# Performance work log

Hardware: AMD Instinct MI355X
Metric: run time of the kernel (lower is better)

The kernel has to match this reference:

```python
import jax, jax.numpy as jnp
import numpy as np

ALPHA = 1.702
LIMIT = 7.0


def setup_inputs() -> dict:
    key = jax.random.key(0)
    ks = jax.random.split(key, 6)
    T, H, D, E = 8192, 1024, 1024, 8
    hidden_states = jax.random.normal(ks[0], (T, H), dtype=jnp.float32)
    routing_weights = jax.random.uniform(ks[1], (T, E), dtype=jnp.float32)
    # 0.02 scale keeps activations in a sane range (original uses raw randn params)
    gate_up_proj = jax.random.normal(ks[2], (E, H, 2 * D), dtype=jnp.float32) * 0.02
    gate_up_proj_bias = jax.random.normal(ks[3], (E, 2 * D), dtype=jnp.float32) * 0.02
    down_proj = jax.random.normal(ks[4], (E, D, H), dtype=jnp.float32) * 0.02
    down_proj_bias = jax.random.normal(ks[5], (E, H), dtype=jnp.float32) * 0.02
    return {
        "hidden_states": hidden_states,
        "routing_weights": routing_weights,
        "gate_up_proj": gate_up_proj,
        "gate_up_proj_bias": gate_up_proj_bias,
        "down_proj": down_proj,
        "down_proj_bias": down_proj_bias,
    }


def reference(hidden_states, routing_weights, gate_up_proj, gate_up_proj_bias,
              down_proj, down_proj_bias):
    # hidden_states: [T, H]; routing_weights: [T, E] (batch_size == T in the torch code)
    B, H = hidden_states.shape[0], hidden_states.shape[-1]
    hs = hidden_states.reshape(-1, H)  # [T, H]
    # all-experts batched GEMM: [E, T, 2D]
    gate_up = jnp.einsum('th,ehd->etd', hs, gate_up_proj) + gate_up_proj_bias[:, None, :]
    gate = jnp.minimum(gate_up[..., ::2], LIMIT)          # [E, T, D]
    up = jnp.clip(gate_up[..., 1::2], -LIMIT, LIMIT)      # [E, T, D]
    glu = gate * jax.nn.sigmoid(gate * ALPHA)
    # down projection: [E, T, H]
    next_states = jnp.einsum('etd,edh->eth', (up + 1.0) * glu, down_proj) \
        + down_proj_bias[:, None, :]
    # routing-weighted combine over experts: [T, H]
    out = jnp.einsum('eth,te->th', next_states, routing_weights)
    return out.reshape(B, -1, H)  # [T, 1, H], matching final .view(batch_size, -1, hidden)
```

## Files before the change

kernel.cpp:

```cpp
#include <hip/hip_runtime.h>
#include <hip/hip_bf16.h>

#define T_DIM 8192
#define H_DIM 1024
#define D_DIM 1024
#define E_DIM 8
#define TWO_D 2048
#define K2 8192

#define ALPHA_C 1.702f
#define LIMIT_C 7.0f

typedef __attribute__((ext_vector_type(8))) short s8v;
typedef __attribute__((ext_vector_type(4))) float f4v;

__device__ __forceinline__ void g2l16(const void* g, void* l) {
    __builtin_amdgcn_global_load_lds((const __attribute__((address_space(1))) void*)g,
                                     (__attribute__((address_space(3))) void*)l, 16, 0, 0);
}

__device__ __forceinline__ unsigned short f2bf(float f) {
    __hip_bfloat16 h = __float2bfloat16(f);
    return __builtin_bit_cast(unsigned short, h);
}


__global__ void f32_to_bf16_kernel(const float* __restrict__ in,
                                   unsigned short* __restrict__ out, size_t n) {
    size_t i = ((size_t)blockIdx.x * blockDim.x + threadIdx.x) * 4;
    if (i + 3 < n) {
        float4 v = *(const float4*)(in + i);
        ushort4 o;
        o.x = f2bf(v.x); o.y = f2bf(v.y); o.z = f2bf(v.z); o.w = f2bf(v.w);
        *(ushort4*)(out + i) = o;
    }
}

__global__ void transpose_conv_kernel(const float* __restrict__ in,
                                      unsigned short* __restrict__ out,
                                      int cols, size_t ibs, size_t obs, size_t ors,
                                      int remap) {
    __shared__ float t[32][33];
    const int b = blockIdx.z;
    const int c0 = blockIdx.x * 32, r0 = blockIdx.y * 32;
    const int tx = threadIdx.x & 31, ty = threadIdx.x >> 5;
    const float* ip = in + (size_t)b * ibs;
    #pragma unroll
    for (int i = 0; i < 4; ++i)
        t[ty + i * 8][tx] = ip[(size_t)(r0 + ty + i * 8) * cols + c0 + tx];
    __syncthreads();
    unsigned short* op = out + (size_t)b * obs;
    #pragma unroll
    for (int i = 0; i < 4; ++i) {
        int c = c0 + ty + i * 8;
        int nc = remap ? ((c & ~31) + ((c & 1) << 4) + ((c >> 1) & 15)) : c;
        op[(size_t)nc * ors + r0 + tx] = f2bf(t[tx][ty + i * 8]);
    }
}


__global__ __launch_bounds__(256, 2) void gemm1_kernel(
    const short* __restrict__ Ag0,
    const short* __restrict__ Bg0,
    const float* __restrict__ b1,
    const float* __restrict__ rw,
    __hip_bfloat16* __restrict__ act2)
{
    const int e = blockIdx.z;
    const int mBase = blockIdx.x * 128;
    const int nBase = blockIdx.y * 128;
    const int tid = threadIdx.x;
    const int lane = tid & 63;
    const int wave = tid >> 6;
    const int wm = wave >> 1, wn = wave & 1;
    const int cq = lane & 15, quad = lane >> 4;

    __shared__ __align__(16) short As[128 * 64];
    __shared__ __align__(16) short Bs[128 * 64];

    const short* Ag = Ag0 + (size_t)mBase * H_DIM;
    const short* Bg = Bg0 + ((size_t)e * TWO_D + nBase) * H_DIM;

    f4v acc[4][4];
    #pragma unroll
    for (int mt = 0; mt < 4; ++mt)
        #pragma unroll
        for (int nt = 0; nt < 4; ++nt)
            acc[mt][nt] = (f4v){0.f, 0.f, 0.f, 0.f};

    const int srow8 = lane >> 3;
    const int gco = ((lane & 7) ^ srow8) * 8;
    const int cq7 = cq & 7;

    for (int k0 = 0; k0 < H_DIM; k0 += 64) {
        #pragma unroll
        for (int i = 0; i < 4; ++i) {
            const int r = wave * 32 + i * 8 + srow8;
            g2l16(Ag + (size_t)r * H_DIM + k0 + gco, As + (wave * 32 + i * 8) * 64);
            g2l16(Bg + (size_t)r * H_DIM + k0 + gco, Bs + (wave * 32 + i * 8) * 64);
        }
        __syncthreads();
        #pragma unroll
        for (int h = 0; h < 2; ++h) {
            s8v af[4], bf[4];
            const int pc = (((h << 2) + quad) ^ cq7) * 8;
            #pragma unroll
            for (int i = 0; i < 4; ++i) {
                af[i] = *(const s8v*)(As + (wm * 64 + i * 16 + cq) * 64 + pc);
                bf[i] = *(const s8v*)(Bs + (wn * 64 + i * 16 + cq) * 64 + pc);
            }
            #pragma unroll
            for (int mt = 0; mt < 4; ++mt)
                #pragma unroll
                for (int nt = 0; nt < 4; ++nt)
                    acc[mt][nt] = __builtin_amdgcn_mfma_f32_16x16x32_bf16(
                        af[mt], bf[nt], acc[mt][nt], 0, 0, 0);
        }
        __syncthreads();
    }

    float rwv[4][4];
    #pragma unroll
    for (int mt = 0; mt < 4; ++mt)
        #pragma unroll
        for (int r = 0; r < 4; ++r)
            rwv[mt][r] = rw[(size_t)(mBase + wm * 64 + mt * 16 + quad * 4 + r) * E_DIM + e];

    #pragma unroll
    for (int p = 0; p < 2; ++p) {
        const int j = (((nBase + wn * 64 + p * 32) >> 5) << 4) + cq;
        const float gb = b1[(size_t)e * TWO_D + 2 * j];
        const float ub = b1[(size_t)e * TWO_D + 2 * j + 1];
        #pragma unroll
        for (int mt = 0; mt < 4; ++mt) {
            #pragma unroll
            for (int r = 0; r < 4; ++r) {
                float gate = acc[mt][2 * p][r] + gb;
                float up   = acc[mt][2 * p + 1][r] + ub;
                gate = fminf(gate, LIMIT_C);
                up = fminf(fmaxf(up, -LIMIT_C), LIMIT_C);
                float glu = gate / (1.f + __expf(-ALPHA_C * gate));
                float a = (up + 1.f) * glu * rwv[mt][r];
                const int row = mBase + wm * 64 + mt * 16 + quad * 4 + r;
                act2[(size_t)row * K2 + (size_t)e * D_DIM + j] = __float2bfloat16(a);
            }
        }
    }
}


#define FEN asm volatile("" ::: "memory")
#define BARR { FEN; __builtin_amdgcn_s_barrier(); FEN; }
#define VMW0 asm volatile("s_waitcnt vmcnt(0)" ::: "memory")

__global__ __launch_bounds__(256, 2) void gemm2_kernel(
    const short* __restrict__ Ag0,
    const short* __restrict__ Bg0,
    const float* __restrict__ rw,
    const float* __restrict__ b3,
    float* __restrict__ out)
{
    const int id = blockIdx.x;
    const int mBase = (id & 63) * 128;
    const int nBase = (id >> 6) * 128;
    const int tid = threadIdx.x;
    const int lane = tid & 63;
    const int wave = tid >> 6;
    const int wm = wave >> 1, wn = wave & 1;
    const int cq = lane & 15, quad = lane >> 4;

    __shared__ __align__(16) short As[2][128 * 64];
    __shared__ __align__(16) short Bs[2][128 * 64];

    const short* Ag = Ag0 + (size_t)mBase * K2;
    const short* Bg = Bg0 + (size_t)nBase * K2;

    f4v acc[4][4];
    #pragma unroll
    for (int mt = 0; mt < 4; ++mt)
        #pragma unroll
        for (int nt = 0; nt < 4; ++nt)
            acc[mt][nt] = (f4v){0.f, 0.f, 0.f, 0.f};

    const int srow8 = lane >> 3;
    const int gco = ((lane & 7) ^ srow8) * 8;
    const int cq7 = cq & 7;

    #pragma unroll
    for (int i = 0; i < 4; ++i) {
        const int r = wave * 32 + i * 8 + srow8;
        g2l16(Ag + (size_t)r * K2 + 0 + gco, &As[0][(wave * 32 + i * 8) * 64]);
        g2l16(Bg + (size_t)r * K2 + 0 + gco, &Bs[0][(wave * 32 + i * 8) * 64]);
    }
    VMW0;
    BARR;

    int cur = 0;
    #pragma unroll 1
    for (int k0 = 0; k0 < K2; k0 += 64) {
        if (k0 + 64 < K2) {
            #pragma unroll
            for (int i = 0; i < 4; ++i) {
                const int r = wave * 32 + i * 8 + srow8;
                g2l16(Ag + (size_t)r * K2 + k0 + 64 + gco,
                      &As[cur ^ 1][(wave * 32 + i * 8) * 64]);
                g2l16(Bg + (size_t)r * K2 + k0 + 64 + gco,
                      &Bs[cur ^ 1][(wave * 32 + i * 8) * 64]);
            }
        }
        FEN;
        const short* Ab = As[cur];
        const short* Bb = Bs[cur];
        __builtin_amdgcn_s_setprio(1);
        #pragma unroll
        for (int h = 0; h < 2; ++h) {
            s8v af[4], bf[4];
            const int pc = (((h << 2) + quad) ^ cq7) * 8;
            #pragma unroll
            for (int i = 0; i < 4; ++i) {
                af[i] = *(const s8v*)(Ab + (wm * 64 + i * 16 + cq) * 64 + pc);
                bf[i] = *(const s8v*)(Bb + (wn * 64 + i * 16 + cq) * 64 + pc);
            }
            #pragma unroll
            for (int mt = 0; mt < 4; ++mt)
                #pragma unroll
                for (int nt = 0; nt < 4; ++nt)
                    acc[mt][nt] = __builtin_amdgcn_mfma_f32_16x16x32_bf16(
                        af[mt], bf[nt], acc[mt][nt], 0, 0, 0);
        }
        __builtin_amdgcn_s_setprio(0);
        VMW0;
        BARR;
        cur ^= 1;
    }

    #pragma unroll
    for (int mt = 0; mt < 4; ++mt) {
        #pragma unroll
        for (int r = 0; r < 4; ++r) {
            const int row = mBase + wm * 64 + mt * 16 + quad * 4 + r;
            const float4 rwa = *(const float4*)(rw + (size_t)row * E_DIM);
            const float4 rwb = *(const float4*)(rw + (size_t)row * E_DIM + 4);
            #pragma unroll
            for (int nt = 0; nt < 4; ++nt) {
                const int col = nBase + wn * 64 + nt * 16 + cq;
                float bias = rwa.x * b3[0 * H_DIM + col] + rwa.y * b3[1 * H_DIM + col]
                           + rwa.z * b3[2 * H_DIM + col] + rwa.w * b3[3 * H_DIM + col]
                           + rwb.x * b3[4 * H_DIM + col] + rwb.y * b3[5 * H_DIM + col]
                           + rwb.z * b3[6 * H_DIM + col] + rwb.w * b3[7 * H_DIM + col];
                out[(size_t)row * H_DIM + col] = acc[mt][nt][r] + bias;
            }
        }
    }
}


extern "C" void kernel_launch(void* const* d_in, const int* in_sizes, int n_in,
                              void* d_out, int out_size, void* d_ws, size_t ws_size,
                              hipStream_t stream) {
    const float* hs = (const float*)d_in[0];
    const float* rw = (const float*)d_in[1];
    const float* w1 = (const float*)d_in[2];
    const float* b1 = (const float*)d_in[3];
    const float* w3 = (const float*)d_in[4];
    const float* b3 = (const float*)d_in[5];
    float* out = (float*)d_out;

    char* ws = (char*)d_ws;
    unsigned short* hsb  = (unsigned short*)(ws);
    unsigned short* w1b  = (unsigned short*)(ws + ((size_t)16 << 20));
    unsigned short* w3b  = (unsigned short*)(ws + ((size_t)48 << 20));
    unsigned short* act2 = (unsigned short*)(ws + ((size_t)64 << 20));

    {
        size_t n = (size_t)T_DIM * H_DIM;
        f32_to_bf16_kernel<<<dim3(n / (256 * 4)), dim3(256), 0, stream>>>(hs, hsb, n);
    }
    transpose_conv_kernel<<<dim3(TWO_D / 32, H_DIM / 32, E_DIM), dim3(256), 0, stream>>>(
        w1, w1b, TWO_D, (size_t)H_DIM * TWO_D, (size_t)TWO_D * H_DIM, (size_t)H_DIM, 1);
    transpose_conv_kernel<<<dim3(H_DIM / 32, D_DIM / 32, E_DIM), dim3(256), 0, stream>>>(
        w3, w3b, H_DIM, (size_t)D_DIM * H_DIM, (size_t)D_DIM, (size_t)K2, 0);
    gemm1_kernel<<<dim3(T_DIM / 128, TWO_D / 128, E_DIM), dim3(256), 0, stream>>>(
        (const short*)hsb, (const short*)w1b, b1, rw, (__hip_bfloat16*)act2);
    gemm2_kernel<<<dim3(512), dim3(256), 0, stream>>>(
        (const short*)act2, (const short*)w3b, rw, b3, out);
}
```

Baseline: 577.4 us.

## Pre-tile and pre-swizzle GEMM2 operands, enlarge GEMM2 tile to 256x128

gemm1 now writes the activation into a tiled 128x64 layout with an XOR swizzle already applied, and a new transpose kernel writes w3 into the same tiled swizzled layout. Each tile stage of gemm2 is then one contiguous 16 KB region, loaded with simple linear global-to-LDS copies. gemm2 switches to 512-thread blocks covering 256x128 output tiles, so each B tile is reused across more rows and the grid drops to 256 blocks. The risks are lower occupancy (one block per CU) and gemm1 writes that are more scattered within a tile.

```diff
diff --git a/kernel.cpp b/kernel.cpp
--- a/kernel.cpp
+++ b/kernel.cpp
@@ -23,6 +23,10 @@
     __hip_bfloat16 h = __float2bfloat16(f);
     return __builtin_bit_cast(unsigned short, h);
 }
+
+#define FEN asm volatile("" ::: "memory")
+#define BARR { FEN; __builtin_amdgcn_s_barrier(); FEN; }
+#define VMW0 asm volatile("s_waitcnt vmcnt(0)" ::: "memory")
 
 
 __global__ void f32_to_bf16_kernel(const float* __restrict__ in,
@@ -58,13 +62,36 @@
     }
 }
 
+__global__ void transpose_w3_tiled_kernel(const float* __restrict__ in,
+                                          unsigned short* __restrict__ out) {
+    __shared__ float t[32][33];
+    const int e = blockIdx.z;
+    const int c0 = blockIdx.x * 32;
+    const int r0 = blockIdx.y * 32;
+    const int tx = threadIdx.x & 31, ty = threadIdx.x >> 5;
+    const float* ip = in + (size_t)e * D_DIM * H_DIM;
+    #pragma unroll
+    for (int i = 0; i < 4; ++i)
+        t[ty + i * 8][tx] = ip[(size_t)(r0 + ty + i * 8) * H_DIM + c0 + tx];
+    __syncthreads();
+    #pragma unroll
+    for (int i = 0; i < 4; ++i) {
+        const int hcol = c0 + ty + i * 8;
+        const int kk = e * D_DIM + r0 + tx;
+        const int nt = hcol >> 7, rIn = hcol & 127;
+        const int kt = kk >> 6, c = kk & 63;
+        out[((size_t)nt * 128 + kt) * 8192 + rIn * 64 + (c ^ ((rIn & 7) << 3))] =
+            f2bf(t[tx][ty + i * 8]);
+    }
+}
+
 
 __global__ __launch_bounds__(256, 2) void gemm1_kernel(
     const short* __restrict__ Ag0,
     const short* __restrict__ Bg0,
     const float* __restrict__ b1,
     const float* __restrict__ rw,
-    __hip_bfloat16* __restrict__ act2)
+    unsigned short* __restrict__ act2t)
 {
     const int e = blockIdx.z;
     const int mBase = blockIdx.x * 128;
@@ -126,11 +153,15 @@
         for (int r = 0; r < 4; ++r)
             rwv[mt][r] = rw[(size_t)(mBase + wm * 64 + mt * 16 + quad * 4 + r) * E_DIM + e];
 
+    const int kt_blk = e * 16 + (nBase >> 7);
+    unsigned short* tb = act2t + ((size_t)blockIdx.x * 128 + kt_blk) * 8192;
+
     #pragma unroll
     for (int p = 0; p < 2; ++p) {
         const int j = (((nBase + wn * 64 + p * 32) >> 5) << 4) + cq;
         const float gb = b1[(size_t)e * TWO_D + 2 * j];
         const float ub = b1[(size_t)e * TWO_D + 2 * j + 1];
+        const int c = wn * 32 + p * 16 + cq;
         #pragma unroll
         for (int mt = 0; mt < 4; ++mt) {
             #pragma unroll
@@ -141,39 +172,33 @@
                 up = fminf(fmaxf(up, -LIMIT_C), LIMIT_C);
                 float glu = gate / (1.f + __expf(-ALPHA_C * gate));
                 float a = (up + 1.f) * glu * rwv[mt][r];
-                const int row = mBase + wm * 64 + mt * 16 + quad * 4 + r;
-                act2[(size_t)row * K2 + (size_t)e * D_DIM + j] = __float2bfloat16(a);
+                const int rIn = wm * 64 + mt * 16 + quad * 4 + r;
+                tb[rIn * 64 + (c ^ ((rIn & 7) << 3))] = f2bf(a);
             }
         }
     }
 }
 
 
-#define FEN asm volatile("" ::: "memory")
-#define BARR { FEN; __builtin_amdgcn_s_barrier(); FEN; }
-#define VMW0 asm volatile("s_waitcnt vmcnt(0)" ::: "memory")
-
-__global__ __launch_bounds__(256, 2) void gemm2_kernel(
-    const short* __restrict__ Ag0,
-    const short* __restrict__ Bg0,
+__global__ __launch_bounds__(512, 1) void gemm2_kernel(
+    const short* __restrict__ At,
+    const short* __restrict__ Bt,
     const float* __restrict__ rw,
     const float* __restrict__ b3,
     float* __restrict__ out)
 {
     const int id = blockIdx.x;
-    const int mBase = (id & 63) * 128;
-    const int nBase = (id >> 6) * 128;
+    const int mIdx = id & 31;
+    const int nIdx = id >> 5;
     const int tid = threadIdx.x;
     const int lane = tid & 63;
     const int wave = tid >> 6;
     const int wm = wave >> 1, wn = wave & 1;
     const int cq = lane & 15, quad = lane >> 4;
-
-    __shared__ __align__(16) short As[2][128 * 64];
+    const int cq7 = cq & 7;
+
+    __shared__ __align__(16) short As[2][256 * 64];
     __shared__ __align__(16) short Bs[2][128 * 64];
-
-    const short* Ag = Ag0 + (size_t)mBase * K2;
-    const short* Bg = Bg0 + (size_t)nBase * K2;
 
     f4v acc[4][4];
     #pragma unroll
@@ -182,32 +207,32 @@
         for (int nt = 0; nt < 4; ++nt)
             acc[mt][nt] = (f4v){0.f, 0.f, 0.f, 0.f};
 
-    const int srow8 = lane >> 3;
-    const int gco = ((lane & 7) ^ srow8) * 8;
-    const int cq7 = cq & 7;
-
-    #pragma unroll
-    for (int i = 0; i < 4; ++i) {
-        const int r = wave * 32 + i * 8 + srow8;
-        g2l16(Ag + (size_t)r * K2 + 0 + gco, &As[0][(wave * 32 + i * 8) * 64]);
-        g2l16(Bg + (size_t)r * K2 + 0 + gco, &Bs[0][(wave * 32 + i * 8) * 64]);
-    }
+    const int lane8 = lane * 8;
+
+#define G2STAGE(KT, BUF)                                                          \
+    { const size_t _kt = (size_t)(KT);                                            \
+      _Pragma("unroll")                                                           \
+      for (int i = 0; i < 4; ++i) {                                               \
+          const int R = wave * 32 + i * 8;                                        \
+          const short* _s = At + ((size_t)(2 * mIdx + (R >> 7)) * 128 + _kt) * 8192 \
+                          + (R & 127) * 64 + lane8;                               \
+          g2l16(_s, &As[BUF][R * 64]);                                            \
+      }                                                                           \
+      _Pragma("unroll")                                                           \
+      for (int i = 0; i < 2; ++i) {                                               \
+          const int R = wave * 16 + i * 8;                                        \
+          const short* _s = Bt + ((size_t)nIdx * 128 + _kt) * 8192 + R * 64 + lane8; \
+          g2l16(_s, &Bs[BUF][R * 64]);                                            \
+      } }
+
+    G2STAGE(0, 0);
     VMW0;
     BARR;
 
     int cur = 0;
     #pragma unroll 1
-    for (int k0 = 0; k0 < K2; k0 += 64) {
-        if (k0 + 64 < K2) {
-            #pragma unroll
-            for (int i = 0; i < 4; ++i) {
-                const int r = wave * 32 + i * 8 + srow8;
-                g2l16(Ag + (size_t)r * K2 + k0 + 64 + gco,
-                      &As[cur ^ 1][(wave * 32 + i * 8) * 64]);
-                g2l16(Bg + (size_t)r * K2 + k0 + 64 + gco,
-                      &Bs[cur ^ 1][(wave * 32 + i * 8) * 64]);
-            }
-        }
+    for (int kt = 0; kt < 128; ++kt) {
+        if (kt + 1 < 128) { G2STAGE(kt + 1, cur ^ 1); }
         FEN;
         const short* Ab = As[cur];
         const short* Bb = Bs[cur];
@@ -234,6 +259,8 @@
         cur ^= 1;
     }
 
+    const int mBase = mIdx * 256;
+    const int nBase = nIdx * 128;
     #pragma unroll
     for (int mt = 0; mt < 4; ++mt) {
         #pragma unroll
@@ -267,10 +294,10 @@
     float* out = (float*)d_out;
 
     char* ws = (char*)d_ws;
-    unsigned short* hsb  = (unsigned short*)(ws);
-    unsigned short* w1b  = (unsigned short*)(ws + ((size_t)16 << 20));
-    unsigned short* w3b  = (unsigned short*)(ws + ((size_t)48 << 20));
-    unsigned short* act2 = (unsigned short*)(ws + ((size_t)64 << 20));
+    unsigned short* hsb   = (unsigned short*)(ws);
+    unsigned short* w1b   = (unsigned short*)(ws + ((size_t)16 << 20));
+    unsigned short* w3t   = (unsigned short*)(ws + ((size_t)48 << 20));
+    unsigned short* act2t = (unsigned short*)(ws + ((size_t)64 << 20));
 
     {
         size_t n = (size_t)T_DIM * H_DIM;
@@ -278,10 +305,10 @@
     }
     transpose_conv_kernel<<<dim3(TWO_D / 32, H_DIM / 32, E_DIM), dim3(256), 0, stream>>>(
         w1, w1b, TWO_D, (size_t)H_DIM * TWO_D, (size_t)TWO_D * H_DIM, (size_t)H_DIM, 1);
-    transpose_conv_kernel<<<dim3(H_DIM / 32, D_DIM / 32, E_DIM), dim3(256), 0, stream>>>(
-        w3, w3b, H_DIM, (size_t)D_DIM * H_DIM, (size_t)D_DIM, (size_t)K2, 0);
+    transpose_w3_tiled_kernel<<<dim3(H_DIM / 32, D_DIM / 32, E_DIM), dim3(256), 0, stream>>>(
+        w3, w3t);
     gemm1_kernel<<<dim3(T_DIM / 128, TWO_D / 128, E_DIM), dim3(256), 0, stream>>>(
-        (const short*)hsb, (const short*)w1b, b1, rw, (__hip_bfloat16*)act2);
-    gemm2_kernel<<<dim3(512), dim3(256), 0, stream>>>(
-        (const short*)act2, (const short*)w3b, rw, b3, out);
-}
+        (const short*)hsb, (const short*)w1b, b1, rw, act2t);
+    gemm2_kernel<<<dim3(256), dim3(512), 0, stream>>>(
+        (const short*)act2t, (const short*)w3t, rw, b3, out);
+}
```

Result: slower. 614.0 us (+6.3%).
